# Kernel tuning notes

Measured on AMD Instinct MI355X. Metric: run time of the kernel, lower is better.

The kernel has to match this reference:

```python
import jax, jax.numpy as jnp
import numpy as np

N, IN_DIM, HID = 8192, 128, 64
LEAKY_SLOPE = 0.2
MASK_VAL = -9e15


def lstm_step(x, W_ih, W_hh, b_ih, b_hh, h0, c0):
    # PyTorch LSTM single time step, gate order i, f, g, o
    gates = x @ W_ih.T + b_ih + h0 @ W_hh.T + b_hh
    i, f, g, o = jnp.split(gates, 4, axis=-1)
    c = jax.nn.sigmoid(f) * c0 + jax.nn.sigmoid(i) * jnp.tanh(g)
    h = jax.nn.sigmoid(o) * jnp.tanh(c)
    return h, c


def setup_inputs() -> dict:
    key = jax.random.key(0)
    ks = jax.random.split(key, 10)
    sc = 0.05
    x = jax.random.normal(ks[0], (N, IN_DIM), jnp.float32)
    adj = jax.random.randint(ks[1], (N, N), 0, 2).astype(jnp.float32)
    fea_W = jax.random.normal(ks[2], (IN_DIM, HID), jnp.float32) * sc
    fea_b = jnp.zeros((HID,), jnp.float32)
    gat_W = jax.random.normal(ks[3], (HID, IN_DIM), jnp.float32) * sc
    gat_a = jax.random.normal(ks[4], (2 * IN_DIM,), jnp.float32) * sc
    enc_W_ih = jax.random.normal(ks[5], (4 * HID, IN_DIM), jnp.float32) * sc
    enc_W_hh = jax.random.normal(ks[6], (4 * HID, HID), jnp.float32) * sc
    enc_b_ih = jnp.zeros((4 * HID,), jnp.float32)
    enc_b_hh = jnp.zeros((4 * HID,), jnp.float32)
    dec_W_ih = jax.random.normal(ks[7], (4 * IN_DIM, HID), jnp.float32) * sc
    dec_W_hh = jax.random.normal(ks[8], (4 * IN_DIM, IN_DIM), jnp.float32) * sc
    dec_b_ih = jnp.zeros((4 * IN_DIM,), jnp.float32)
    dec_b_hh = jnp.zeros((4 * IN_DIM,), jnp.float32)
    return dict(x=x, adj=adj, fea_W=fea_W, fea_b=fea_b, gat_W=gat_W, gat_a=gat_a,
                enc_W_ih=enc_W_ih, enc_W_hh=enc_W_hh, enc_b_ih=enc_b_ih, enc_b_hh=enc_b_hh,
                dec_W_ih=dec_W_ih, dec_W_hh=dec_W_hh, dec_b_ih=dec_b_ih, dec_b_hh=dec_b_hh)


def reference(x, adj, fea_W, fea_b, gat_W, gat_a,
              enc_W_ih, enc_W_hh, enc_b_ih, enc_b_hh,
              dec_W_ih, dec_W_hh, dec_b_ih, dec_b_hh):
    # structure branch: Linear + ReLU then GAT layer
    structure = jax.nn.relu(x @ fea_W + fea_b)            # [N, HID]
    Wh = structure @ gat_W                                # [N, IN_DIM]
    a1, a2 = gat_a[:IN_DIM], gat_a[IN_DIM:]
    e = jax.nn.leaky_relu((Wh @ a1)[:, None] + (Wh @ a2)[None, :], LEAKY_SLOPE)  # [N, N]
    scores = jnp.where(adj > 0, e, MASK_VAL)
    att = jax.nn.softmax(scores, axis=1)
    emb = jax.nn.elu(att @ Wh)                            # [N, IN_DIM]
    # attribute branch: seq_len=1 encoder/decoder LSTM with zero init states
    h0e = jnp.zeros((N, HID), x.dtype)
    h_enc, _ = lstm_step(x, enc_W_ih, enc_W_hh, enc_b_ih, enc_b_hh, h0e, h0e)
    h0d = jnp.zeros((N, IN_DIM), x.dtype)
    att_adj, _ = lstm_step(h_enc, dec_W_ih, dec_W_hh, dec_b_ih, dec_b_hh, h0d, h0d)  # [N, IN_DIM]
    con_adj = emb @ emb.T                                 # [N, N]
    return con_adj, att_adj
```

## Files before the change

kernel.cpp:

```cpp
#include <hip/hip_runtime.h>
#include <hip/hip_bf16.h>

typedef __hip_bfloat16 bf16_t;
typedef short bf16x8 __attribute__((ext_vector_type(8)));
typedef float f32x4 __attribute__((ext_vector_type(4)));

#define NROW 8192
#define LEAKY 0.2f

__device__ __forceinline__ float b2f(bf16_t v){ return __bfloat162float(v); }
__device__ __forceinline__ unsigned short f2b(float f){
  union { bf16_t h; unsigned short u; } cv; cv.h = __float2bfloat16(f); return cv.u;
}
__device__ __forceinline__ float sigf(float v){ return 1.0f / (1.0f + __expf(-v)); }

__global__ void k_probe(const unsigned short* __restrict__ x_raw, int* __restrict__ flag)
{
  const int lane = threadIdx.x;
  int cnt = 0;
  for (int k = lane; k < 512; k += 64){
    const int e = (x_raw[k] >> 7) & 0xff;
    cnt += (e >= 120 && e <= 130) ? 1 : 0;
  }
  #pragma unroll
  for (int s = 1; s < 64; s <<= 1) cnt += __shfl_xor(cnt, s, 64);
  if (lane == 0) flag[0] = (cnt < 384) ? 1 : 0;
}

__global__ __launch_bounds__(256) void k_cvt(
    const void* __restrict__ encW, const void* __restrict__ decW,
    const int* __restrict__ flag,
    unsigned short* __restrict__ encWb, unsigned short* __restrict__ decWb)
{
  const int idx = blockIdx.x*256 + threadIdx.x;
  const int isf32 = flag[0];
  if (idx < 32768){
    float v = isf32 ? ((const float*)encW)[idx] : b2f(((const bf16_t*)encW)[idx]);
    encWb[idx] = f2b(v);
  } else {
    const int j = idx - 32768;
    float v = isf32 ? ((const float*)decW)[j] : b2f(((const bf16_t*)decW)[j]);
    decWb[j] = f2b(v);
  }
}

__global__ __launch_bounds__(256) void k_feamask(
    const void* __restrict__ x, const void* __restrict__ adj,
    const void* __restrict__ fea_W, const void* __restrict__ fea_b,
    const void* __restrict__ gat_W, const void* __restrict__ gat_a,
    const int* __restrict__ flag,
    unsigned short* __restrict__ Whb_p, float* __restrict__ s1, float* __restrict__ s2,
    unsigned short* __restrict__ xb, unsigned char* __restrict__ mask8)
{
  const int r = blockIdx.x, tid = threadIdx.x;
  const int isf32 = flag[0];

  float4 mv0, mv1, mv2, mv3, mv4, mv5, mv6, mv7;
  bf16x8 bv0, bv1, bv2, bv3;
  if (isf32){
    const float4* arow = (const float4*)((const float*)adj + (size_t)r*NROW);
    mv0 = arow[(size_t)tid*2];         mv1 = arow[(size_t)tid*2+1];
    mv2 = arow[(size_t)(tid+256)*2];   mv3 = arow[(size_t)(tid+256)*2+1];
    mv4 = arow[(size_t)(tid+512)*2];   mv5 = arow[(size_t)(tid+512)*2+1];
    mv6 = arow[(size_t)(tid+768)*2];   mv7 = arow[(size_t)(tid+768)*2+1];
  } else {
    const unsigned short* arow = (const unsigned short*)adj + (size_t)r*NROW;
    bv0 = *(const bf16x8*)(arow + (size_t)tid*8);
    bv1 = *(const bf16x8*)(arow + (size_t)(tid+256)*8);
    bv2 = *(const bf16x8*)(arow + (size_t)(tid+512)*8);
    bv3 = *(const bf16x8*)(arow + (size_t)(tid+768)*8);
  }

  if (tid < 64){
    const int l = tid;
    float x0, x1;
    if (isf32){
      const float* xr = (const float*)x + (size_t)r*128;
      x0 = xr[l]; x1 = xr[l+64];
    } else {
      const bf16_t* xr = (const bf16_t*)x + (size_t)r*128;
      x0 = b2f(xr[l]); x1 = b2f(xr[l+64]);
    }
    xb[(size_t)r*128 + l]      = f2b(x0);
    xb[(size_t)r*128 + 64 + l] = f2b(x1);

    float acc = isf32 ? ((const float*)fea_b)[l] : b2f(((const bf16_t*)fea_b)[l]);
    if (isf32){
      const float* W = (const float*)fea_W;
      #pragma unroll
      for (int d=0; d<64; ++d) acc = fmaf(__shfl(x0, d, 64), W[d*64+l], acc);
      #pragma unroll
      for (int d=0; d<64; ++d) acc = fmaf(__shfl(x1, d, 64), W[(d+64)*64+l], acc);
    } else {
      const bf16_t* W = (const bf16_t*)fea_W;
      #pragma unroll
      for (int d=0; d<64; ++d) acc = fmaf(__shfl(x0, d, 64), b2f(W[d*64+l]), acc);
      #pragma unroll
      for (int d=0; d<64; ++d) acc = fmaf(__shfl(x1, d, 64), b2f(W[(d+64)*64+l]), acc);
    }
    const float stv = fmaxf(acc, 0.0f);

    float w0 = 0.f, w1 = 0.f;
    if (isf32){
      const float* W = (const float*)gat_W;
      #pragma unroll
      for (int d=0; d<64; ++d){
        const float sd = __shfl(stv, d, 64);
        w0 = fmaf(sd, W[d*128+l],    w0);
        w1 = fmaf(sd, W[d*128+64+l], w1);
      }
    } else {
      const bf16_t* W = (const bf16_t*)gat_W;
      #pragma unroll
      for (int d=0; d<64; ++d){
        const float sd = __shfl(stv, d, 64);
        w0 = fmaf(sd, b2f(W[d*128+l]),    w0);
        w1 = fmaf(sd, b2f(W[d*128+64+l]), w1);
      }
    }

    const size_t pbase = (size_t)(r >> 3)*1024 + (r & 7);
    Whb_p[pbase + (size_t)l*8]        = f2b(w0);
    Whb_p[pbase + (size_t)(l+64)*8]   = f2b(w1);

    float a10, a11, a20, a21;
    if (isf32){
      const float* A = (const float*)gat_a;
      a10 = A[l]; a11 = A[l+64]; a20 = A[128+l]; a21 = A[192+l];
    } else {
      const bf16_t* A = (const bf16_t*)gat_a;
      a10 = b2f(A[l]); a11 = b2f(A[l+64]); a20 = b2f(A[128+l]); a21 = b2f(A[192+l]);
    }
    float r1 = w0*a10 + w1*a11;
    float r2 = w0*a20 + w1*a21;
    #pragma unroll
    for (int s=1; s<64; s<<=1){ r1 += __shfl_xor(r1, s, 64); r2 += __shfl_xor(r2, s, 64); }
    if (l == 0){ s1[r] = r1; s2[r] = r2; }
  }

  if (isf32){
    const float4 va[8] = { mv0, mv1, mv2, mv3, mv4, mv5, mv6, mv7 };
    #pragma unroll
    for (int k=0;k<4;++k){
      const float4 v0 = va[2*k], v1 = va[2*k+1];
      unsigned int m =
          (unsigned int)(v0.x>0.f)      | ((unsigned int)(v0.y>0.f)<<1) |
          ((unsigned int)(v0.z>0.f)<<2) | ((unsigned int)(v0.w>0.f)<<3) |
          ((unsigned int)(v1.x>0.f)<<4) | ((unsigned int)(v1.y>0.f)<<5) |
          ((unsigned int)(v1.z>0.f)<<6) | ((unsigned int)(v1.w>0.f)<<7);
      mask8[(size_t)r*1024 + tid + k*256] = (unsigned char)m;
    }
  } else {
    const bf16x8 vb[4] = { bv0, bv1, bv2, bv3 };
    #pragma unroll
    for (int k=0;k<4;++k){
      unsigned int m = 0;
      #pragma unroll
      for (int j=0;j<8;++j){
        union { short s; unsigned short u; } cv; cv.s = vb[k][j];
        union { unsigned short u; bf16_t h; } cv2; cv2.u = cv.u;
        m |= ((unsigned int)(b2f(cv2.h) > 0.f)) << j;
      }
      mask8[(size_t)r*1024 + tid + k*256] = (unsigned char)m;
    }
  }
}

__global__ __launch_bounds__(256) void k_enc2(
    const unsigned short* __restrict__ xb, const unsigned short* __restrict__ Wb,
    const void* __restrict__ b_ih, const void* __restrict__ b_hh,
    const int* __restrict__ flag, unsigned short* __restrict__ h_enc_b)
{
  __shared__ float g_lds[32][257];
  const int tid = threadIdx.x, lane = tid & 63, wv = tid >> 6;
  const int quad = lane >> 4, nn = lane & 15;
  const int rowbase = blockIdx.x * 32;
  const int rows_off = (wv & 1) * 16;
  const int col_off  = (wv >> 1) * 128;

  f32x4 acc[8];
  #pragma unroll
  for (int t=0;t<8;++t) acc[t] = (f32x4){0.f,0.f,0.f,0.f};

  #pragma unroll
  for (int ks=0; ks<4; ++ks){
    const int kb = ks*32 + quad*8;
    bf16x8 afrag = *(const bf16x8*)(xb + (size_t)(rowbase + rows_off + nn)*128 + kb);
    #pragma unroll
    for (int t=0;t<8;++t){
      bf16x8 bfrag = *(const bf16x8*)(Wb + (size_t)(col_off + t*16 + nn)*128 + kb);
      acc[t] = __builtin_amdgcn_mfma_f32_16x16x32_bf16(afrag, bfrag, acc[t], 0, 0, 0);
    }
  }
  #pragma unroll
  for (int t=0;t<8;++t)
    #pragma unroll
    for (int r=0;r<4;++r)
      g_lds[rows_off + quad*4 + r][col_off + t*16 + nn] = acc[t][r];
  __syncthreads();

  const int isf32 = flag[0];
  #pragma unroll
  for (int k=0;k<8;++k){
    const int idx = tid + k*256;
    const int r = idx >> 6, hid = idx & 63;
    float bi, bg, bo;
    if (isf32){
      const float* bi1 = (const float*)b_ih; const float* bi2 = (const float*)b_hh;
      bi = bi1[hid]     + bi2[hid];
      bg = bi1[128+hid] + bi2[128+hid];
      bo = bi1[192+hid] + bi2[192+hid];
    } else {
      const bf16_t* bi1 = (const bf16_t*)b_ih; const bf16_t* bi2 = (const bf16_t*)b_hh;
      bi = b2f(bi1[hid])     + b2f(bi2[hid]);
      bg = b2f(bi1[128+hid]) + b2f(bi2[128+hid]);
      bo = b2f(bi1[192+hid]) + b2f(bi2[192+hid]);
    }
    const float gi = g_lds[r][hid]     + bi;
    const float gg = g_lds[r][128+hid] + bg;
    const float go = g_lds[r][192+hid] + bo;
    const float c = tanhf(gg) * sigf(gi);
    const float h = tanhf(c)  * sigf(go);
    h_enc_b[(size_t)(rowbase + r)*64 + hid] = f2b(h);
  }
}

__global__ __launch_bounds__(256) void k_dec2(
    const unsigned short* __restrict__ hb, const unsigned short* __restrict__ Wb,
    const void* __restrict__ b_ih, const void* __restrict__ b_hh,
    const int* __restrict__ flag, void* __restrict__ d_out)
{
  __shared__ float g_lds[16][517];
  const int tid = threadIdx.x, lane = tid & 63, wv = tid >> 6;
  const int quad = lane >> 4, nn = lane & 15;
  const int rowbase = blockIdx.x * 16;
  const int col_off = wv * 128;

  f32x4 acc[8];
  #pragma unroll
  for (int t=0;t<8;++t) acc[t] = (f32x4){0.f,0.f,0.f,0.f};

  #pragma unroll
  for (int ks=0; ks<2; ++ks){
    const int kb = ks*32 + quad*8;
    bf16x8 afrag = *(const bf16x8*)(hb + (size_t)(rowbase + nn)*64 + kb);
    #pragma unroll
    for (int t=0;t<8;++t){
      bf16x8 bfrag = *(const bf16x8*)(Wb + (size_t)(col_off + t*16 + nn)*64 + kb);
      acc[t] = __builtin_amdgcn_mfma_f32_16x16x32_bf16(afrag, bfrag, acc[t], 0, 0, 0);
    }
  }
  #pragma unroll
  for (int t=0;t<8;++t)
    #pragma unroll
    for (int r=0;r<4;++r)
      g_lds[quad*4 + r][col_off + t*16 + nn] = acc[t][r];
  __syncthreads();

  const int isf32 = flag[0];
  #pragma unroll
  for (int k=0;k<8;++k){
    const int idx = tid + k*256;
    const int r = idx >> 7, col = idx & 127;
    float bi, bg, bo;
    if (isf32){
      const float* b1 = (const float*)b_ih; const float* b2 = (const float*)b_hh;
      bi = b1[col]     + b2[col];
      bg = b1[256+col] + b2[256+col];
      bo = b1[384+col] + b2[384+col];
    } else {
      const bf16_t* b1 = (const bf16_t*)b_ih; const bf16_t* b2v = (const bf16_t*)b_hh;
      bi = b2f(b1[col])     + b2f(b2v[col]);
      bg = b2f(b1[256+col]) + b2f(b2v[256+col]);
      bo = b2f(b1[384+col]) + b2f(b2v[384+col]);
    }
    const float gi = g_lds[r][col]     + bi;
    const float gg = g_lds[r][256+col] + bg;
    const float go = g_lds[r][384+col] + bo;
    const float c = tanhf(gg) * sigf(gi);
    const float h = tanhf(c)  * sigf(go);
    const size_t oidx = (size_t)NROW*NROW + (size_t)(rowbase + r)*128 + col;
    if (isf32) ((float*)d_out)[oidx] = h;
    else       ((unsigned short*)d_out)[oidx] = f2b(h);
  }
}

__global__ __launch_bounds__(512) void k_attn(
    const unsigned char* __restrict__ mask8, const unsigned short* __restrict__ Whb_p,
    const float* __restrict__ s1g, const float* __restrict__ s2g,
    unsigned short* __restrict__ emb_p)
{
  __shared__ float C_lds[8][16*128];
  __shared__ float dn_lds[8][16];
  const int tid  = threadIdx.x;
  const int lane = tid & 63;
  const int wv   = tid >> 6;
  const int quad = lane >> 4;
  const int mrow = lane & 15;
  const int rowbase = blockIdx.x * 16;
  const float s1row = s1g[rowbase + mrow];
  const unsigned char* mrow_ptr = mask8 + (size_t)(rowbase + mrow) * 1024;

  f32x4 acc[8];
  #pragma unroll
  for (int t=0;t<8;++t) acc[t] = (f32x4){0.f,0.f,0.f,0.f};
  float dn = 0.f;

  const int jbeg = wv * 1024;
  for (int j0 = jbeg; j0 < jbeg + 1024; j0 += 128){
    uint4 mw = *(const uint4*)(mrow_ptr + (j0 >> 3));
    #pragma unroll
    for (int t4=0; t4<4; ++t4){
      const unsigned int wbits = ((const unsigned int*)&mw)[t4];
      const unsigned int mb = (wbits >> (8*quad)) & 0xffu;
      const int kb = j0 + t4*32 + quad*8;
      float4 s2a = *(const float4*)(s2g + kb);
      float4 s2b = *(const float4*)(s2g + kb + 4);
      const float sv[8] = { s2a.x, s2a.y, s2a.z, s2a.w, s2b.x, s2b.y, s2b.z, s2b.w };
      bf16x8 afrag;
      #pragma unroll
      for (int b=0;b<8;++b){
        float v = s1row + sv[b];
        v = (v > 0.f) ? v : LEAKY * v;
        const float e = __expf(v);
        const float p = (mb & (1u<<b)) ? e : 0.f;
        dn += p;
        afrag[b] = (short)f2b(p);
      }
      const unsigned short* wb = Whb_p + (size_t)(kb >> 3)*1024 + mrow*8;
      #pragma unroll
      for (int t=0;t<8;++t){
        bf16x8 bfrag = *(const bf16x8*)(wb + t*128);
        acc[t] = __builtin_amdgcn_mfma_f32_16x16x32_bf16(afrag, bfrag, acc[t], 0, 0, 0);
      }
    }
  }

  #pragma unroll
  for (int t=0;t<8;++t){
    #pragma unroll
    for (int r=0;r<4;++r)
      C_lds[wv][(quad*4+r)*128 + t*16 + mrow] = acc[t][r];
  }
  dn += __shfl_xor(dn, 16, 64);
  dn += __shfl_xor(dn, 32, 64);
  if (lane < 16) dn_lds[wv][lane] = dn;
  __syncthreads();

  for (int idx = tid; idx < 16*128; idx += 512){
    const int m = idx >> 7;
    const int d = idx & 127;
    float v = C_lds[0][idx] + C_lds[1][idx] + C_lds[2][idx] + C_lds[3][idx]
            + C_lds[4][idx] + C_lds[5][idx] + C_lds[6][idx] + C_lds[7][idx];
    const float den = dn_lds[0][m] + dn_lds[1][m] + dn_lds[2][m] + dn_lds[3][m]
                    + dn_lds[4][m] + dn_lds[5][m] + dn_lds[6][m] + dn_lds[7][m];
    v /= den;
    v = (v > 0.f) ? v : (__expf(v) - 1.f);
    emb_p[(size_t)(d >> 3)*65536 + (size_t)(rowbase + m)*8 + (d & 7)] = f2b(v);
  }
}

__global__ __launch_bounds__(256) void k_out(
    const unsigned short* __restrict__ emb_p, const int* __restrict__ flag,
    void* __restrict__ d_out)
{
  const int tid  = threadIdx.x;
  const int lane = tid & 63, wv = tid >> 6;
  const int quad = lane >> 4, nn = lane & 15;
  const int i0 = blockIdx.y * 128 + wv * 32;
  const int j0 = blockIdx.x * 64;

  f32x4 acc[2][4];
  #pragma unroll
  for (int a=0;a<2;++a)
    #pragma unroll
    for (int b=0;b<4;++b) acc[a][b] = (f32x4){0.f,0.f,0.f,0.f};

  #pragma unroll
  for (int ks=0; ks<4; ++ks){
    const int kb = ks*32 + quad*8;
    const unsigned short* base = emb_p + (size_t)(kb >> 3)*65536;
    bf16x8 a0 = *(const bf16x8*)(base + (size_t)(i0 + nn)*8);
    bf16x8 a1 = *(const bf16x8*)(base + (size_t)(i0 + 16 + nn)*8);
    #pragma unroll
    for (int t=0;t<4;++t){
      bf16x8 b = *(const bf16x8*)(base + (size_t)(j0 + t*16 + nn)*8);
      acc[0][t] = __builtin_amdgcn_mfma_f32_16x16x32_bf16(a0, b, acc[0][t], 0, 0, 0);
      acc[1][t] = __builtin_amdgcn_mfma_f32_16x16x32_bf16(a1, b, acc[1][t], 0, 0, 0);
    }
  }

  const int isf32 = flag[0];
  if (isf32){
    float* out = (float*)d_out;
    #pragma unroll
    for (int mi=0; mi<2; ++mi)
      #pragma unroll
      for (int t=0;t<4;++t)
        #pragma unroll
        for (int r=0;r<4;++r)
          out[(size_t)(i0 + mi*16 + quad*4 + r)*NROW + j0 + t*16 + nn] = acc[mi][t][r];
  } else {
    unsigned short* out = (unsigned short*)d_out;
    #pragma unroll
    for (int mi=0; mi<2; ++mi)
      #pragma unroll
      for (int t=0;t<4;++t)
        #pragma unroll
        for (int r=0;r<4;++r)
          out[(size_t)(i0 + mi*16 + quad*4 + r)*NROW + j0 + t*16 + nn] = f2b(acc[mi][t][r]);
  }
}

extern "C" void kernel_launch(void* const* d_in, const int* in_sizes, int n_in,
                              void* d_out, int out_size, void* d_ws, size_t ws_size,
                              hipStream_t stream)
{
  (void)in_sizes; (void)n_in; (void)out_size; (void)ws_size;
  const void* x        = d_in[0];
  const void* adj      = d_in[1];
  const void* fea_W    = d_in[2];
  const void* fea_b    = d_in[3];
  const void* gat_W    = d_in[4];
  const void* gat_a    = d_in[5];
  const void* enc_W_ih = d_in[6];
  const void* enc_b_ih = d_in[8];
  const void* enc_b_hh = d_in[9];
  const void* dec_W_ih = d_in[10];
  const void* dec_b_ih = d_in[12];
  const void* dec_b_hh = d_in[13];

  char* ws = (char*)d_ws;
  unsigned short* Whb_p   = (unsigned short*)ws;
  unsigned short* emb_p   = (unsigned short*)(ws + (2u<<20));
  unsigned short* xb      = (unsigned short*)(ws + (4u<<20));
  unsigned short* h_enc_b = (unsigned short*)(ws + (6u<<20));
  unsigned char*  mask8   = (unsigned char*) (ws + (7u<<20));
  float* s1    = (float*)(ws + (15u<<20));
  float* s2    = (float*)(ws + (15u<<20) + 32768);
  unsigned short* encWb = (unsigned short*)(ws + (15u<<20) + 65536);
  unsigned short* decWb = (unsigned short*)(ws + (15u<<20) + 65536 + 65536);
  int* flag = (int*)(ws + (15u<<20) + 3*65536);

  k_probe<<<1, 64, 0, stream>>>((const unsigned short*)x, flag);
  k_cvt<<<256, 256, 0, stream>>>(enc_W_ih, dec_W_ih, flag, encWb, decWb);
  k_feamask<<<NROW, 256, 0, stream>>>(x, adj, fea_W, fea_b, gat_W, gat_a, flag,
                                      Whb_p, s1, s2, xb, mask8);
  k_enc2<<<256, 256, 0, stream>>>(xb, encWb, enc_b_ih, enc_b_hh, flag, h_enc_b);
  k_dec2<<<512, 256, 0, stream>>>(h_enc_b, decWb, dec_b_ih, dec_b_hh, flag, d_out);
  k_attn<<<512, 512, 0, stream>>>(mask8, Whb_p, s1, s2, emb_p);
  k_out<<<dim3(128, 64), 256, 0, stream>>>(emb_p, flag, d_out);
}
```

Baseline: 592.2 us.

## Fuse dtype probe, weight conversion, and LSTM branch into fewer launches

Every block in the prep kernel now derives the fp32/bf16 flag inline, so the separate probe launch goes away. The weight-conversion work moves into 64 extra blocks of the feature/mask kernel. The encoder and decoder LSTM steps become one code path: the encoder's h is kept in swizzled shared memory and never written to global. That path runs as extra blocks of the attention kernel, so the LSTM branch overlaps the GAT attention work and four kernel launches are removed. In exchange, the attention kernel's shared memory and register footprint now also covers the LSTM path, which can limit occupancy.

Result: slower. 658.1 us (+11.1%).

```diff
diff --git a/kernel.cpp b/kernel.cpp
--- a/kernel.cpp
+++ b/kernel.cpp
@@ -14,46 +14,54 @@
 }
 __device__ __forceinline__ float sigf(float v){ return 1.0f / (1.0f + __expf(-v)); }
 
-__global__ void k_probe(const unsigned short* __restrict__ x_raw, int* __restrict__ flag)
+__device__ __forceinline__ int flag_is_f32(const void* x)
 {
-  const int lane = threadIdx.x;
+  const unsigned short* xr = (const unsigned short*)x;
+  const int lane = threadIdx.x & 63;
+  const ushort4 a = ((const ushort4*)xr)[lane*2];
+  const ushort4 b = ((const ushort4*)xr)[lane*2+1];
+  const unsigned short vs[8] = {a.x,a.y,a.z,a.w,b.x,b.y,b.z,b.w};
   int cnt = 0;
-  for (int k = lane; k < 512; k += 64){
-    const int e = (x_raw[k] >> 7) & 0xff;
-    cnt += (e >= 120 && e <= 130) ? 1 : 0;
-  }
   #pragma unroll
-  for (int s = 1; s < 64; s <<= 1) cnt += __shfl_xor(cnt, s, 64);
-  if (lane == 0) flag[0] = (cnt < 384) ? 1 : 0;
-}
-
-__global__ __launch_bounds__(256) void k_cvt(
-    const void* __restrict__ encW, const void* __restrict__ decW,
-    const int* __restrict__ flag,
-    unsigned short* __restrict__ encWb, unsigned short* __restrict__ decWb)
-{
-  const int idx = blockIdx.x*256 + threadIdx.x;
-  const int isf32 = flag[0];
-  if (idx < 32768){
-    float v = isf32 ? ((const float*)encW)[idx] : b2f(((const bf16_t*)encW)[idx]);
-    encWb[idx] = f2b(v);
-  } else {
-    const int j = idx - 32768;
-    float v = isf32 ? ((const float*)decW)[j] : b2f(((const bf16_t*)decW)[j]);
-    decWb[j] = f2b(v);
-  }
-}
-
-__global__ __launch_bounds__(256) void k_feamask(
+  for (int j=0;j<8;++j){ const int e=(vs[j]>>7)&0xff; cnt += (e>=120 && e<=130) ? 1 : 0; }
+  #pragma unroll
+  for (int s=1;s<64;s<<=1) cnt += __shfl_xor(cnt, s, 64);
+  return (cnt < 384) ? 1 : 0;
+}
+
+__global__ __launch_bounds__(256) void k_prep(
     const void* __restrict__ x, const void* __restrict__ adj,
     const void* __restrict__ fea_W, const void* __restrict__ fea_b,
     const void* __restrict__ gat_W, const void* __restrict__ gat_a,
-    const int* __restrict__ flag,
+    const void* __restrict__ encW, const void* __restrict__ decW,
     unsigned short* __restrict__ Whb_p, float* __restrict__ s1, float* __restrict__ s2,
-    unsigned short* __restrict__ xb, unsigned char* __restrict__ mask8)
+    unsigned short* __restrict__ xb, unsigned char* __restrict__ mask8,
+    unsigned short* __restrict__ encWb, unsigned short* __restrict__ decWb,
+    int* __restrict__ flag)
 {
-  const int r = blockIdx.x, tid = threadIdx.x;
-  const int isf32 = flag[0];
+  const int tid = threadIdx.x;
+  const int isf32 = flag_is_f32(x);
+
+  if (blockIdx.x >= NROW){
+    const int bb = blockIdx.x - NROW;
+    if (bb == 0 && tid == 0) flag[0] = isf32;
+    const int base = (bb*256 + tid)*4;
+    #pragma unroll
+    for (int j=0;j<4;++j){
+      const int idx = base + j;
+      if (idx < 32768){
+        float v = isf32 ? ((const float*)encW)[idx] : b2f(((const bf16_t*)encW)[idx]);
+        encWb[idx] = f2b(v);
+      } else {
+        const int jj = idx - 32768;
+        float v = isf32 ? ((const float*)decW)[jj] : b2f(((const bf16_t*)decW)[jj]);
+        decWb[jj] = f2b(v);
+      }
+    }
+    return;
+  }
+
+  const int r = blockIdx.x;
 
   float4 mv0, mv1, mv2, mv3, mv4, mv5, mv6, mv7;
   bf16x8 bv0, bv1, bv2, bv3;
@@ -120,8 +128,8 @@
     }
 
     const size_t pbase = (size_t)(r >> 3)*1024 + (r & 7);
-    Whb_p[pbase + (size_t)l*8]        = f2b(w0);
-    Whb_p[pbase + (size_t)(l+64)*8]   = f2b(w1);
+    Whb_p[pbase + (size_t)l*8]      = f2b(w0);
+    Whb_p[pbase + (size_t)(l+64)*8] = f2b(w1);
 
     float a10, a11, a20, a21;
     if (isf32){
@@ -166,197 +174,188 @@
   }
 }
 
-__global__ __launch_bounds__(256) void k_enc2(
-    const unsigned short* __restrict__ xb, const unsigned short* __restrict__ Wb,
-    const void* __restrict__ b_ih, const void* __restrict__ b_hh,
-    const int* __restrict__ flag, unsigned short* __restrict__ h_enc_b)
-{
-  __shared__ float g_lds[32][257];
-  const int tid = threadIdx.x, lane = tid & 63, wv = tid >> 6;
-  const int quad = lane >> 4, nn = lane & 15;
-  const int rowbase = blockIdx.x * 32;
-  const int rows_off = (wv & 1) * 16;
-  const int col_off  = (wv >> 1) * 128;
-
-  f32x4 acc[8];
-  #pragma unroll
-  for (int t=0;t<8;++t) acc[t] = (f32x4){0.f,0.f,0.f,0.f};
-
-  #pragma unroll
-  for (int ks=0; ks<4; ++ks){
-    const int kb = ks*32 + quad*8;
-    bf16x8 afrag = *(const bf16x8*)(xb + (size_t)(rowbase + rows_off + nn)*128 + kb);
-    #pragma unroll
-    for (int t=0;t<8;++t){
-      bf16x8 bfrag = *(const bf16x8*)(Wb + (size_t)(col_off + t*16 + nn)*128 + kb);
-      acc[t] = __builtin_amdgcn_mfma_f32_16x16x32_bf16(afrag, bfrag, acc[t], 0, 0, 0);
-    }
-  }
-  #pragma unroll
-  for (int t=0;t<8;++t)
-    #pragma unroll
-    for (int r=0;r<4;++r)
-      g_lds[rows_off + quad*4 + r][col_off + t*16 + nn] = acc[t][r];
-  __syncthreads();
-
-  const int isf32 = flag[0];
-  #pragma unroll
-  for (int k=0;k<8;++k){
-    const int idx = tid + k*256;
-    const int r = idx >> 6, hid = idx & 63;
-    float bi, bg, bo;
-    if (isf32){
-      const float* bi1 = (const float*)b_ih; const float* bi2 = (const float*)b_hh;
-      bi = bi1[hid]     + bi2[hid];
-      bg = bi1[128+hid] + bi2[128+hid];
-      bo = bi1[192+hid] + bi2[192+hid];
-    } else {
-      const bf16_t* bi1 = (const bf16_t*)b_ih; const bf16_t* bi2 = (const bf16_t*)b_hh;
-      bi = b2f(bi1[hid])     + b2f(bi2[hid]);
-      bg = b2f(bi1[128+hid]) + b2f(bi2[128+hid]);
-      bo = b2f(bi1[192+hid]) + b2f(bi2[192+hid]);
-    }
-    const float gi = g_lds[r][hid]     + bi;
-    const float gg = g_lds[r][128+hid] + bg;
-    const float go = g_lds[r][192+hid] + bo;
-    const float c = tanhf(gg) * sigf(gi);
-    const float h = tanhf(c)  * sigf(go);
-    h_enc_b[(size_t)(rowbase + r)*64 + hid] = f2b(h);
-  }
-}
-
-__global__ __launch_bounds__(256) void k_dec2(
-    const unsigned short* __restrict__ hb, const unsigned short* __restrict__ Wb,
-    const void* __restrict__ b_ih, const void* __restrict__ b_hh,
-    const int* __restrict__ flag, void* __restrict__ d_out)
-{
-  __shared__ float g_lds[16][517];
-  const int tid = threadIdx.x, lane = tid & 63, wv = tid >> 6;
-  const int quad = lane >> 4, nn = lane & 15;
-  const int rowbase = blockIdx.x * 16;
-  const int col_off = wv * 128;
-
-  f32x4 acc[8];
-  #pragma unroll
-  for (int t=0;t<8;++t) acc[t] = (f32x4){0.f,0.f,0.f,0.f};
-
-  #pragma unroll
-  for (int ks=0; ks<2; ++ks){
-    const int kb = ks*32 + quad*8;
-    bf16x8 afrag = *(const bf16x8*)(hb + (size_t)(rowbase + nn)*64 + kb);
-    #pragma unroll
-    for (int t=0;t<8;++t){
-      bf16x8 bfrag = *(const bf16x8*)(Wb + (size_t)(col_off + t*16 + nn)*64 + kb);
-      acc[t] = __builtin_amdgcn_mfma_f32_16x16x32_bf16(afrag, bfrag, acc[t], 0, 0, 0);
-    }
-  }
-  #pragma unroll
-  for (int t=0;t<8;++t)
-    #pragma unroll
-    for (int r=0;r<4;++r)
-      g_lds[quad*4 + r][col_off + t*16 + nn] = acc[t][r];
-  __syncthreads();
-
-  const int isf32 = flag[0];
-  #pragma unroll
-  for (int k=0;k<8;++k){
-    const int idx = tid + k*256;
-    const int r = idx >> 7, col = idx & 127;
-    float bi, bg, bo;
-    if (isf32){
-      const float* b1 = (const float*)b_ih; const float* b2 = (const float*)b_hh;
-      bi = b1[col]     + b2[col];
-      bg = b1[256+col] + b2[256+col];
-      bo = b1[384+col] + b2[384+col];
-    } else {
-      const bf16_t* b1 = (const bf16_t*)b_ih; const bf16_t* b2v = (const bf16_t*)b_hh;
-      bi = b2f(b1[col])     + b2f(b2v[col]);
-      bg = b2f(b1[256+col]) + b2f(b2v[256+col]);
-      bo = b2f(b1[384+col]) + b2f(b2v[384+col]);
-    }
-    const float gi = g_lds[r][col]     + bi;
-    const float gg = g_lds[r][256+col] + bg;
-    const float go = g_lds[r][384+col] + bo;
-    const float c = tanhf(gg) * sigf(gi);
-    const float h = tanhf(c)  * sigf(go);
-    const size_t oidx = (size_t)NROW*NROW + (size_t)(rowbase + r)*128 + col;
-    if (isf32) ((float*)d_out)[oidx] = h;
-    else       ((unsigned short*)d_out)[oidx] = f2b(h);
-  }
-}
-
-__global__ __launch_bounds__(512) void k_attn(
+__global__ __launch_bounds__(512) void k_main(
     const unsigned char* __restrict__ mask8, const unsigned short* __restrict__ Whb_p,
     const float* __restrict__ s1g, const float* __restrict__ s2g,
-    unsigned short* __restrict__ emb_p)
+    unsigned short* __restrict__ emb_p,
+    const unsigned short* __restrict__ xb,
+    const unsigned short* __restrict__ encWb, const unsigned short* __restrict__ decWb,
+    const void* __restrict__ eb_ih, const void* __restrict__ eb_hh,
+    const void* __restrict__ db_ih, const void* __restrict__ db_hh,
+    const int* __restrict__ flag, void* __restrict__ d_out)
 {
   __shared__ float C_lds[8][16*128];
   __shared__ float dn_lds[8][16];
+  __shared__ unsigned short h_sh[64*64];
+
   const int tid  = threadIdx.x;
   const int lane = tid & 63;
   const int wv   = tid >> 6;
   const int quad = lane >> 4;
-  const int mrow = lane & 15;
-  const int rowbase = blockIdx.x * 16;
-  const float s1row = s1g[rowbase + mrow];
-  const unsigned char* mrow_ptr = mask8 + (size_t)(rowbase + mrow) * 1024;
-
-  f32x4 acc[8];
-  #pragma unroll
-  for (int t=0;t<8;++t) acc[t] = (f32x4){0.f,0.f,0.f,0.f};
-  float dn = 0.f;
-
-  const int jbeg = wv * 1024;
-  for (int j0 = jbeg; j0 < jbeg + 1024; j0 += 128){
-    uint4 mw = *(const uint4*)(mrow_ptr + (j0 >> 3));
-    #pragma unroll
-    for (int t4=0; t4<4; ++t4){
-      const unsigned int wbits = ((const unsigned int*)&mw)[t4];
-      const unsigned int mb = (wbits >> (8*quad)) & 0xffu;
-      const int kb = j0 + t4*32 + quad*8;
-      float4 s2a = *(const float4*)(s2g + kb);
-      float4 s2b = *(const float4*)(s2g + kb + 4);
-      const float sv[8] = { s2a.x, s2a.y, s2a.z, s2a.w, s2b.x, s2b.y, s2b.z, s2b.w };
-      bf16x8 afrag;
-      #pragma unroll
-      for (int b=0;b<8;++b){
-        float v = s1row + sv[b];
-        v = (v > 0.f) ? v : LEAKY * v;
-        const float e = __expf(v);
-        const float p = (mb & (1u<<b)) ? e : 0.f;
-        dn += p;
-        afrag[b] = (short)f2b(p);
-      }
-      const unsigned short* wb = Whb_p + (size_t)(kb >> 3)*1024 + mrow*8;
-      #pragma unroll
-      for (int t=0;t<8;++t){
-        bf16x8 bfrag = *(const bf16x8*)(wb + t*128);
-        acc[t] = __builtin_amdgcn_mfma_f32_16x16x32_bf16(afrag, bfrag, acc[t], 0, 0, 0);
-      }
-    }
-  }
-
-  #pragma unroll
-  for (int t=0;t<8;++t){
-    #pragma unroll
-    for (int r=0;r<4;++r)
-      C_lds[wv][(quad*4+r)*128 + t*16 + mrow] = acc[t][r];
-  }
-  dn += __shfl_xor(dn, 16, 64);
-  dn += __shfl_xor(dn, 32, 64);
-  if (lane < 16) dn_lds[wv][lane] = dn;
-  __syncthreads();
-
-  for (int idx = tid; idx < 16*128; idx += 512){
-    const int m = idx >> 7;
-    const int d = idx & 127;
-    float v = C_lds[0][idx] + C_lds[1][idx] + C_lds[2][idx] + C_lds[3][idx]
-            + C_lds[4][idx] + C_lds[5][idx] + C_lds[6][idx] + C_lds[7][idx];
-    const float den = dn_lds[0][m] + dn_lds[1][m] + dn_lds[2][m] + dn_lds[3][m]
-                    + dn_lds[4][m] + dn_lds[5][m] + dn_lds[6][m] + dn_lds[7][m];
-    v /= den;
-    v = (v > 0.f) ? v : (__expf(v) - 1.f);
-    emb_p[(size_t)(d >> 3)*65536 + (size_t)(rowbase + m)*8 + (d & 7)] = f2b(v);
+
+  if (blockIdx.x < 512){
+    const int mrow = lane & 15;
+    const int rowbase = blockIdx.x * 16;
+    const float s1row = s1g[rowbase + mrow];
+    const unsigned char* mrow_ptr = mask8 + (size_t)(rowbase + mrow) * 1024;
+
+    f32x4 acc[8];
+    #pragma unroll
+    for (int t=0;t<8;++t) acc[t] = (f32x4){0.f,0.f,0.f,0.f};
+    float dn = 0.f;
+
+    const int jbeg = wv * 1024;
+    for (int j0 = jbeg; j0 < jbeg + 1024; j0 += 128){
+      uint4 mw = *(const uint4*)(mrow_ptr + (j0 >> 3));
+      #pragma unroll
+      for (int t4=0; t4<4; ++t4){
+        const unsigned int wbits = ((const unsigned int*)&mw)[t4];
+        const unsigned int mb = (wbits >> (8*quad)) & 0xffu;
+        const int kb = j0 + t4*32 + quad*8;
+        float4 s2a = *(const float4*)(s2g + kb);
+        float4 s2b = *(const float4*)(s2g + kb + 4);
+        const float sv[8] = { s2a.x, s2a.y, s2a.z, s2a.w, s2b.x, s2b.y, s2b.z, s2b.w };
+        bf16x8 afrag;
+        #pragma unroll
+        for (int b=0;b<8;++b){
+          float v = s1row + sv[b];
+          v = (v > 0.f) ? v : LEAKY * v;
+          const float e = __expf(v);
+          const float p = (mb & (1u<<b)) ? e : 0.f;
+          dn += p;
+          afrag[b] = (short)f2b(p);
+        }
+        const unsigned short* wb = Whb_p + (size_t)(kb >> 3)*1024 + mrow*8;
+        #pragma unroll
+        for (int t=0;t<8;++t){
+          bf16x8 bfrag = *(const bf16x8*)(wb + t*128);
+          acc[t] = __builtin_amdgcn_mfma_f32_16x16x32_bf16(afrag, bfrag, acc[t], 0, 0, 0);
+        }
+      }
+    }
+
+    #pragma unroll
+    for (int t=0;t<8;++t){
+      #pragma unroll
+      for (int r=0;r<4;++r)
+        C_lds[wv][(quad*4+r)*128 + t*16 + mrow] = acc[t][r];
+    }
+    dn += __shfl_xor(dn, 16, 64);
+    dn += __shfl_xor(dn, 32, 64);
+    if (lane < 16) dn_lds[wv][lane] = dn;
+    __syncthreads();
+
+    for (int idx = tid; idx < 16*128; idx += 512){
+      const int m = idx >> 7;
+      const int d = idx & 127;
+      float v = C_lds[0][idx] + C_lds[1][idx] + C_lds[2][idx] + C_lds[3][idx]
+              + C_lds[4][idx] + C_lds[5][idx] + C_lds[6][idx] + C_lds[7][idx];
+      const float den = dn_lds[0][m] + dn_lds[1][m] + dn_lds[2][m] + dn_lds[3][m]
+                      + dn_lds[4][m] + dn_lds[5][m] + dn_lds[6][m] + dn_lds[7][m];
+      v /= den;
+      v = (v > 0.f) ? v : (__expf(v) - 1.f);
+      emb_p[(size_t)(d >> 3)*65536 + (size_t)(rowbase + m)*8 + (d & 7)] = f2b(v);
+    }
+  } else {
+    const int b = blockIdx.x - 512;
+    const int nn = lane & 15;
+    const int rg = (wv & 3) * 16;
+    const int ch = wv >> 2;
+    const int rowbase = b * 64;
+    const int isf32 = flag[0];
+
+    f32x4 eacc[3][2];
+    #pragma unroll
+    for (int g=0; g<3; ++g)
+      #pragma unroll
+      for (int tt=0; tt<2; ++tt) eacc[g][tt] = (f32x4){0.f,0.f,0.f,0.f};
+    const int egb[3] = {0, 128, 192};
+
+    #pragma unroll
+    for (int ks=0; ks<4; ++ks){
+      const int kb = ks*32 + quad*8;
+      bf16x8 af = *(const bf16x8*)(xb + (size_t)(rowbase + rg + nn)*128 + kb);
+      #pragma unroll
+      for (int g=0; g<3; ++g)
+        #pragma unroll
+        for (int tt=0; tt<2; ++tt){
+          const int bcol = egb[g] + ch*32 + tt*16 + nn;
+          bf16x8 bf = *(const bf16x8*)(encWb + (size_t)bcol*128 + kb);
+          eacc[g][tt] = __builtin_amdgcn_mfma_f32_16x16x32_bf16(af, bf, eacc[g][tt], 0, 0, 0);
+        }
+    }
+    #pragma unroll
+    for (int tt=0; tt<2; ++tt){
+      const int c = ch*32 + tt*16 + nn;
+      float bi, bg, bo;
+      if (isf32){
+        const float* b1 = (const float*)eb_ih; const float* b2 = (const float*)eb_hh;
+        bi = b1[c]+b2[c]; bg = b1[128+c]+b2[128+c]; bo = b1[192+c]+b2[192+c];
+      } else {
+        const bf16_t* b1 = (const bf16_t*)eb_ih; const bf16_t* b2 = (const bf16_t*)eb_hh;
+        bi = b2f(b1[c])+b2f(b2[c]); bg = b2f(b1[128+c])+b2f(b2[128+c]); bo = b2f(b1[192+c])+b2f(b2[192+c]);
+      }
+      #pragma unroll
+      for (int r=0; r<4; ++r){
+        const float gi = eacc[0][tt][r] + bi;
+        const float gg = eacc[1][tt][r] + bg;
+        const float go = eacc[2][tt][r] + bo;
+        const float cc = tanhf(gg) * sigf(gi);
+        const float h  = tanhf(cc) * sigf(go);
+        const int row = rg + quad*4 + r;
+        unsigned int byte = (unsigned int)row*128 + (unsigned int)c*2;
+        byte ^= (unsigned int)(row & 7) << 4;
+        *(unsigned short*)((char*)h_sh + byte) = f2b(h);
+      }
+    }
+    __syncthreads();
+
+    f32x4 dacc[3][4];
+    #pragma unroll
+    for (int g=0; g<3; ++g)
+      #pragma unroll
+      for (int tt=0; tt<4; ++tt) dacc[g][tt] = (f32x4){0.f,0.f,0.f,0.f};
+    const int dgb[3] = {0, 256, 384};
+
+    #pragma unroll
+    for (int ks=0; ks<2; ++ks){
+      const int kb = ks*32 + quad*8;
+      const int arow = rg + nn;
+      unsigned int byte = (unsigned int)arow*128 + (unsigned int)kb*2;
+      byte ^= (unsigned int)(arow & 7) << 4;
+      bf16x8 af = *(const bf16x8*)((const char*)h_sh + byte);
+      #pragma unroll
+      for (int g=0; g<3; ++g)
+        #pragma unroll
+        for (int tt=0; tt<4; ++tt){
+          const int bcol = dgb[g] + ch*64 + tt*16 + nn;
+          bf16x8 bf = *(const bf16x8*)(decWb + (size_t)bcol*64 + kb);
+          dacc[g][tt] = __builtin_amdgcn_mfma_f32_16x16x32_bf16(af, bf, dacc[g][tt], 0, 0, 0);
+        }
+    }
+    #pragma unroll
+    for (int tt=0; tt<4; ++tt){
+      const int col = ch*64 + tt*16 + nn;
+      float bi, bg, bo;
+      if (isf32){
+        const float* b1 = (const float*)db_ih; const float* b2 = (const float*)db_hh;
+        bi = b1[col]+b2[col]; bg = b1[256+col]+b2[256+col]; bo = b1[384+col]+b2[384+col];
+      } else {
+        const bf16_t* b1 = (const bf16_t*)db_ih; const bf16_t* b2 = (const bf16_t*)db_hh;
+        bi = b2f(b1[col])+b2f(b2[col]); bg = b2f(b1[256+col])+b2f(b2[256+col]); bo = b2f(b1[384+col])+b2f(b2[384+col]);
+      }
+      #pragma unroll
+      for (int r=0; r<4; ++r){
+        const float gi = dacc[0][tt][r] + bi;
+        const float gg = dacc[1][tt][r] + bg;
+        const float go = dacc[2][tt][r] + bo;
+        const float cc = tanhf(gg) * sigf(gi);
+        const float h  = tanhf(cc) * sigf(go);
+        const size_t oidx = (size_t)NROW*NROW + (size_t)(rowbase + rg + quad*4 + r)*128 + col;
+        if (isf32) ((float*)d_out)[oidx] = h;
+        else       ((unsigned short*)d_out)[oidx] = f2b(h);
+      }
+    }
   }
 }
 
@@ -434,20 +433,19 @@
   unsigned short* Whb_p   = (unsigned short*)ws;
   unsigned short* emb_p   = (unsigned short*)(ws + (2u<<20));
   unsigned short* xb      = (unsigned short*)(ws + (4u<<20));
-  unsigned short* h_enc_b = (unsigned short*)(ws + (6u<<20));
-  unsigned char*  mask8   = (unsigned char*) (ws + (7u<<20));
-  float* s1    = (float*)(ws + (15u<<20));
-  float* s2    = (float*)(ws + (15u<<20) + 32768);
-  unsigned short* encWb = (unsigned short*)(ws + (15u<<20) + 65536);
-  unsigned short* decWb = (unsigned short*)(ws + (15u<<20) + 65536 + 65536);
-  int* flag = (int*)(ws + (15u<<20) + 3*65536);
-
-  k_probe<<<1, 64, 0, stream>>>((const unsigned short*)x, flag);
-  k_cvt<<<256, 256, 0, stream>>>(enc_W_ih, dec_W_ih, flag, encWb, decWb);
-  k_feamask<<<NROW, 256, 0, stream>>>(x, adj, fea_W, fea_b, gat_W, gat_a, flag,
-                                      Whb_p, s1, s2, xb, mask8);
-  k_enc2<<<256, 256, 0, stream>>>(xb, encWb, enc_b_ih, enc_b_hh, flag, h_enc_b);
-  k_dec2<<<512, 256, 0, stream>>>(h_enc_b, decWb, dec_b_ih, dec_b_hh, flag, d_out);
-  k_attn<<<512, 512, 0, stream>>>(mask8, Whb_p, s1, s2, emb_p);
+  unsigned char*  mask8   = (unsigned char*) (ws + (6u<<20));
+  float* s1    = (float*)(ws + (14u<<20));
+  float* s2    = (float*)(ws + (14u<<20) + 32768);
+  unsigned short* encWb = (unsigned short*)(ws + (14u<<20) + 65536);
+  unsigned short* decWb = (unsigned short*)(ws + (14u<<20) + 65536 + 65536);
+  int* flag = (int*)(ws + (14u<<20) + 3*65536);
+
+  k_prep<<<NROW + 64, 256, 0, stream>>>(x, adj, fea_W, fea_b, gat_W, gat_a,
+                                        enc_W_ih, dec_W_ih,
+                                        Whb_p, s1, s2, xb, mask8, encWb, decWb, flag);
+  k_main<<<512 + 128, 512, 0, stream>>>(mask8, Whb_p, s1, s2, emb_p,
+                                        xb, encWb, decWb,
+                                        enc_b_ih, enc_b_hh, dec_b_ih, dec_b_hh,
+                                        flag, d_out);
   k_out<<<dim3(128, 64), 256, 0, stream>>>(emb_p, flag, d_out);
 }
```

## Batch feature kernel over 8 rows and precompute gat_W·a projections

Applied to the files above, without the earlier changes.

The per-row feature/mask kernel becomes one that handles 8 rows per block. x is staged in shared memory so that fea_W and gat_W loads are reused across rows and all 256 threads do the matmul work, not just 64. The attention scores s1/s2 now come from a precomputed gat_W@a vector, computed in an extra block of the conversion kernel, instead of reducing over Wh. Mask building now packs 32 bits per thread with a per-thread serial loop over 8 rows. The bf16 path uses a bitwise positive test, and the fp32 path's strided per-thread float4 reads may coalesce less well.

Result: slower. 615.4 us (+3.9%).

```diff
diff --git a/kernel.cpp b/kernel.cpp
--- a/kernel.cpp
+++ b/kernel.cpp
@@ -29,11 +29,34 @@
 
 __global__ __launch_bounds__(256) void k_cvt(
     const void* __restrict__ encW, const void* __restrict__ decW,
+    const void* __restrict__ gat_W, const void* __restrict__ gat_a,
     const int* __restrict__ flag,
-    unsigned short* __restrict__ encWb, unsigned short* __restrict__ decWb)
-{
-  const int idx = blockIdx.x*256 + threadIdx.x;
+    unsigned short* __restrict__ encWb, unsigned short* __restrict__ decWb,
+    float* __restrict__ ga1, float* __restrict__ ga2)
+{
+  const int tid = threadIdx.x;
   const int isf32 = flag[0];
+  if (blockIdx.x == 256){
+    if (tid < 128){
+      const int d = tid & 63;
+      const int which = tid >> 6;
+      float acc = 0.f;
+      if (isf32){
+        const float* W = (const float*)gat_W;
+        const float* A = (const float*)gat_a + which*128;
+        #pragma unroll 8
+        for (int c=0; c<128; ++c) acc = fmaf(W[d*128+c], A[c], acc);
+      } else {
+        const bf16_t* W = (const bf16_t*)gat_W;
+        const bf16_t* A = (const bf16_t*)gat_a + which*128;
+        #pragma unroll 8
+        for (int c=0; c<128; ++c) acc = fmaf(b2f(W[d*128+c]), b2f(A[c]), acc);
+      }
+      if (which == 0) ga1[d] = acc; else ga2[d] = acc;
+    }
+    return;
+  }
+  const int idx = blockIdx.x*256 + tid;
   if (idx < 32768){
     float v = isf32 ? ((const float*)encW)[idx] : b2f(((const bf16_t*)encW)[idx]);
     encWb[idx] = f2b(v);
@@ -44,124 +67,129 @@
   }
 }
 
-__global__ __launch_bounds__(256) void k_feamask(
+__global__ __launch_bounds__(256) void k_fea8(
     const void* __restrict__ x, const void* __restrict__ adj,
     const void* __restrict__ fea_W, const void* __restrict__ fea_b,
-    const void* __restrict__ gat_W, const void* __restrict__ gat_a,
+    const void* __restrict__ gat_W,
+    const float* __restrict__ ga1, const float* __restrict__ ga2,
     const int* __restrict__ flag,
     unsigned short* __restrict__ Whb_p, float* __restrict__ s1, float* __restrict__ s2,
     unsigned short* __restrict__ xb, unsigned char* __restrict__ mask8)
 {
-  const int r = blockIdx.x, tid = threadIdx.x;
+  __shared__ float xs[8][128];
+  __shared__ float sts[8][64];
+  const int tid = threadIdx.x;
+  const int rb  = blockIdx.x * 8;
   const int isf32 = flag[0];
 
-  float4 mv0, mv1, mv2, mv3, mv4, mv5, mv6, mv7;
-  bf16x8 bv0, bv1, bv2, bv3;
-  if (isf32){
-    const float4* arow = (const float4*)((const float*)adj + (size_t)r*NROW);
-    mv0 = arow[(size_t)tid*2];         mv1 = arow[(size_t)tid*2+1];
-    mv2 = arow[(size_t)(tid+256)*2];   mv3 = arow[(size_t)(tid+256)*2+1];
-    mv4 = arow[(size_t)(tid+512)*2];   mv5 = arow[(size_t)(tid+512)*2+1];
-    mv6 = arow[(size_t)(tid+768)*2];   mv7 = arow[(size_t)(tid+768)*2+1];
-  } else {
-    const unsigned short* arow = (const unsigned short*)adj + (size_t)r*NROW;
-    bv0 = *(const bf16x8*)(arow + (size_t)tid*8);
-    bv1 = *(const bf16x8*)(arow + (size_t)(tid+256)*8);
-    bv2 = *(const bf16x8*)(arow + (size_t)(tid+512)*8);
-    bv3 = *(const bf16x8*)(arow + (size_t)(tid+768)*8);
-  }
-
-  if (tid < 64){
-    const int l = tid;
-    float x0, x1;
+  {
+    float4 v;
     if (isf32){
-      const float* xr = (const float*)x + (size_t)r*128;
-      x0 = xr[l]; x1 = xr[l+64];
+      v = *(const float4*)((const float*)x + (size_t)rb*128 + tid*4);
     } else {
-      const bf16_t* xr = (const bf16_t*)x + (size_t)r*128;
-      x0 = b2f(xr[l]); x1 = b2f(xr[l+64]);
-    }
-    xb[(size_t)r*128 + l]      = f2b(x0);
-    xb[(size_t)r*128 + 64 + l] = f2b(x1);
-
-    float acc = isf32 ? ((const float*)fea_b)[l] : b2f(((const bf16_t*)fea_b)[l]);
+      const bf16_t* xr = (const bf16_t*)x + (size_t)rb*128 + tid*4;
+      v.x = b2f(xr[0]); v.y = b2f(xr[1]); v.z = b2f(xr[2]); v.w = b2f(xr[3]);
+    }
+    ((float4*)&xs[0][0])[tid] = v;
+    ushort4 o; o.x = f2b(v.x); o.y = f2b(v.y); o.z = f2b(v.z); o.w = f2b(v.w);
+    *(ushort4*)(xb + (size_t)rb*128 + tid*4) = o;
+  }
+  __syncthreads();
+
+  {
+    const int c  = tid & 63;
+    const int wv = tid >> 6;
+    float bcol = isf32 ? ((const float*)fea_b)[c] : b2f(((const bf16_t*)fea_b)[c]);
+    float a0 = bcol, a1v = bcol;
     if (isf32){
       const float* W = (const float*)fea_W;
-      #pragma unroll
-      for (int d=0; d<64; ++d) acc = fmaf(__shfl(x0, d, 64), W[d*64+l], acc);
-      #pragma unroll
-      for (int d=0; d<64; ++d) acc = fmaf(__shfl(x1, d, 64), W[(d+64)*64+l], acc);
+      #pragma unroll 8
+      for (int d=0; d<128; ++d){
+        const float w = W[d*64 + c];
+        a0  = fmaf(xs[2*wv  ][d], w, a0);
+        a1v = fmaf(xs[2*wv+1][d], w, a1v);
+      }
     } else {
       const bf16_t* W = (const bf16_t*)fea_W;
-      #pragma unroll
-      for (int d=0; d<64; ++d) acc = fmaf(__shfl(x0, d, 64), b2f(W[d*64+l]), acc);
-      #pragma unroll
-      for (int d=0; d<64; ++d) acc = fmaf(__shfl(x1, d, 64), b2f(W[(d+64)*64+l]), acc);
-    }
-    const float stv = fmaxf(acc, 0.0f);
-
-    float w0 = 0.f, w1 = 0.f;
+      #pragma unroll 8
+      for (int d=0; d<128; ++d){
+        const float w = b2f(W[d*64 + c]);
+        a0  = fmaf(xs[2*wv  ][d], w, a0);
+        a1v = fmaf(xs[2*wv+1][d], w, a1v);
+      }
+    }
+    a0  = fmaxf(a0, 0.f);
+    a1v = fmaxf(a1v, 0.f);
+    sts[2*wv  ][c] = a0;
+    sts[2*wv+1][c] = a1v;
+
+    const float g1 = ga1[c], g2 = ga2[c];
+    float p10 = a0*g1, p11 = a1v*g1, p20 = a0*g2, p21 = a1v*g2;
+    #pragma unroll
+    for (int s=1; s<64; s<<=1){
+      p10 += __shfl_xor(p10, s, 64); p11 += __shfl_xor(p11, s, 64);
+      p20 += __shfl_xor(p20, s, 64); p21 += __shfl_xor(p21, s, 64);
+    }
+    if ((tid & 63) == 0){
+      s1[rb + 2*wv]     = p10;  s1[rb + 2*wv + 1] = p11;
+      s2[rb + 2*wv]     = p20;  s2[rb + 2*wv + 1] = p21;
+    }
+  }
+  __syncthreads();
+
+  {
+    const int c  = tid & 127;
+    const int rg = tid >> 7;
+    float w0=0.f, w1=0.f, w2=0.f, w3=0.f;
     if (isf32){
       const float* W = (const float*)gat_W;
-      #pragma unroll
+      #pragma unroll 8
       for (int d=0; d<64; ++d){
-        const float sd = __shfl(stv, d, 64);
-        w0 = fmaf(sd, W[d*128+l],    w0);
-        w1 = fmaf(sd, W[d*128+64+l], w1);
+        const float g = W[d*128 + c];
+        w0 = fmaf(sts[rg*4  ][d], g, w0);
+        w1 = fmaf(sts[rg*4+1][d], g, w1);
+        w2 = fmaf(sts[rg*4+2][d], g, w2);
+        w3 = fmaf(sts[rg*4+3][d], g, w3);
       }
     } else {
       const bf16_t* W = (const bf16_t*)gat_W;
-      #pragma unroll
+      #pragma unroll 8
       for (int d=0; d<64; ++d){
-        const float sd = __shfl(stv, d, 64);
-        w0 = fmaf(sd, b2f(W[d*128+l]),    w0);
-        w1 = fmaf(sd, b2f(W[d*128+64+l]), w1);
-      }
-    }
-
-    const size_t pbase = (size_t)(r >> 3)*1024 + (r & 7);
-    Whb_p[pbase + (size_t)l*8]        = f2b(w0);
-    Whb_p[pbase + (size_t)(l+64)*8]   = f2b(w1);
-
-    float a10, a11, a20, a21;
-    if (isf32){
-      const float* A = (const float*)gat_a;
-      a10 = A[l]; a11 = A[l+64]; a20 = A[128+l]; a21 = A[192+l];
-    } else {
-      const bf16_t* A = (const bf16_t*)gat_a;
-      a10 = b2f(A[l]); a11 = b2f(A[l+64]); a20 = b2f(A[128+l]); a21 = b2f(A[192+l]);
-    }
-    float r1 = w0*a10 + w1*a11;
-    float r2 = w0*a20 + w1*a21;
-    #pragma unroll
-    for (int s=1; s<64; s<<=1){ r1 += __shfl_xor(r1, s, 64); r2 += __shfl_xor(r2, s, 64); }
-    if (l == 0){ s1[r] = r1; s2[r] = r2; }
+        const float g = b2f(W[d*128 + c]);
+        w0 = fmaf(sts[rg*4  ][d], g, w0);
+        w1 = fmaf(sts[rg*4+1][d], g, w1);
+        w2 = fmaf(sts[rg*4+2][d], g, w2);
+        w3 = fmaf(sts[rg*4+3][d], g, w3);
+      }
+    }
+    unsigned short* wp = Whb_p + (size_t)(rb >> 3)*1024 + (size_t)c*8 + rg*4;
+    wp[0] = f2b(w0); wp[1] = f2b(w1); wp[2] = f2b(w2); wp[3] = f2b(w3);
   }
 
   if (isf32){
-    const float4 va[8] = { mv0, mv1, mv2, mv3, mv4, mv5, mv6, mv7 };
-    #pragma unroll
-    for (int k=0;k<4;++k){
-      const float4 v0 = va[2*k], v1 = va[2*k+1];
-      unsigned int m =
-          (unsigned int)(v0.x>0.f)      | ((unsigned int)(v0.y>0.f)<<1) |
-          ((unsigned int)(v0.z>0.f)<<2) | ((unsigned int)(v0.w>0.f)<<3) |
-          ((unsigned int)(v1.x>0.f)<<4) | ((unsigned int)(v1.y>0.f)<<5) |
-          ((unsigned int)(v1.z>0.f)<<6) | ((unsigned int)(v1.w>0.f)<<7);
-      mask8[(size_t)r*1024 + tid + k*256] = (unsigned char)m;
+    const float* arow = (const float*)adj + (size_t)rb*NROW;
+    for (int rr=0; rr<8; ++rr){
+      const float4* a4 = (const float4*)(arow + (size_t)rr*NROW) + tid*8;
+      unsigned int m = 0;
+      #pragma unroll
+      for (int j=0;j<8;++j){
+        const float4 v = a4[j];
+        m |= ((unsigned int)(v.x>0.f) | ((unsigned int)(v.y>0.f)<<1) |
+              ((unsigned int)(v.z>0.f)<<2) | ((unsigned int)(v.w>0.f)<<3)) << (j*4);
+      }
+      ((unsigned int*)mask8)[(size_t)(rb+rr)*256 + tid] = m;
     }
   } else {
-    const bf16x8 vb[4] = { bv0, bv1, bv2, bv3 };
-    #pragma unroll
-    for (int k=0;k<4;++k){
+    const unsigned short* arow = (const unsigned short*)adj + (size_t)rb*NROW;
+    for (int rr=0; rr<8; ++rr){
+      const unsigned short* a8 = arow + (size_t)rr*NROW + tid*32;
       unsigned int m = 0;
       #pragma unroll
-      for (int j=0;j<8;++j){
-        union { short s; unsigned short u; } cv; cv.s = vb[k][j];
-        union { unsigned short u; bf16_t h; } cv2; cv2.u = cv.u;
-        m |= ((unsigned int)(b2f(cv2.h) > 0.f)) << j;
-      }
-      mask8[(size_t)r*1024 + tid + k*256] = (unsigned char)m;
+      for (int j=0;j<32;++j){
+        const unsigned short u = a8[j];
+        m |= ((unsigned int)(u > 0 && u < 0x8000)) << j;
+      }
+      ((unsigned int*)mask8)[(size_t)(rb+rr)*256 + tid] = m;
     }
   }
 }
@@ -440,12 +468,15 @@
   float* s2    = (float*)(ws + (15u<<20) + 32768);
   unsigned short* encWb = (unsigned short*)(ws + (15u<<20) + 65536);
   unsigned short* decWb = (unsigned short*)(ws + (15u<<20) + 65536 + 65536);
-  int* flag = (int*)(ws + (15u<<20) + 3*65536);
+  float* ga1 = (float*)(ws + (15u<<20) + 3*65536);
+  float* ga2 = (float*)(ws + (15u<<20) + 3*65536 + 256);
+  int* flag  = (int*) (ws + (15u<<20) + 3*65536 + 512);
 
   k_probe<<<1, 64, 0, stream>>>((const unsigned short*)x, flag);
-  k_cvt<<<256, 256, 0, stream>>>(enc_W_ih, dec_W_ih, flag, encWb, decWb);
-  k_feamask<<<NROW, 256, 0, stream>>>(x, adj, fea_W, fea_b, gat_W, gat_a, flag,
-                                      Whb_p, s1, s2, xb, mask8);
+  k_cvt<<<257, 256, 0, stream>>>(enc_W_ih, dec_W_ih, gat_W, gat_a, flag,
+                                 encWb, decWb, ga1, ga2);
+  k_fea8<<<1024, 256, 0, stream>>>(x, adj, fea_W, fea_b, gat_W, ga1, ga2, flag,
+                                   Whb_p, s1, s2, xb, mask8);
   k_enc2<<<256, 256, 0, stream>>>(xb, encWb, enc_b_ih, enc_b_hh, flag, h_enc_b);
   k_dec2<<<512, 256, 0, stream>>>(h_enc_b, decWb, dec_b_ih, dec_b_hh, flag, d_out);
   k_attn<<<512, 512, 0, stream>>>(mask8, Whb_p, s1, s2, emb_p);
```
